# Optimization experiments

Measured on AMD Instinct MI355X. Metric: run time of the kernel, lower is better.

The kernel has to match this reference:

```python
import jax, jax.numpy as jnp
import numpy as np
from jax import lax

N, T, CH, EMB, H, C = 256, 87, 21, 50, 128, 43  # utterances, max tokens, chars, glove dim, gru hidden, classes


def setup_inputs() -> dict:
    key = jax.random.key(0)
    ks = iter(jax.random.split(key, 40))
    def rn(shape, s=0.1):
        return (jax.random.normal(next(ks), shape) * s).astype(jnp.float32)
    return {
        "token_embeddings": rn((N, T, EMB), 1.0),
        "token_char_embeddings": rn((N, T, CH, EMB), 1.0),
        "conv1_w": rn((T, T, 5, 5)), "conv1_b": rn((T,)),
        "conv2_w": rn((T, T, 5, 5)), "conv2_b": rn((T,)),
        "utt_wih_f": rn((3 * H, 58)), "utt_whh_f": rn((3 * H, H)),
        "utt_bih_f": rn((3 * H,)), "utt_bhh_f": rn((3 * H,)),
        "utt_wih_b": rn((3 * H, 58)), "utt_whh_b": rn((3 * H, H)),
        "utt_bih_b": rn((3 * H,)), "utt_bhh_b": rn((3 * H,)),
        "ctx_w1": rn((H, 2 * H)), "ctx_w2": rn((H, H)), "ctx_b2": rn((H,)), "ctx_w3": rn((H, H)),
        "proj_w": rn((1, 2 * H)), "proj_b": rn((1,)),
        "gx0": rn((2, 2, H)),
        "cg_wih_f": rn((3 * H, 1)), "cg_whh_f": rn((3 * H, H)),
        "cg_bih_f": rn((3 * H,)), "cg_bhh_f": rn((3 * H,)),
        "cg_wih_b": rn((3 * H, 1)), "cg_whh_b": rn((3 * H, H)),
        "cg_bih_b": rn((3 * H,)), "cg_bhh_b": rn((3 * H,)),
        "cls_w1": rn((2 * H, 4 * H)), "cls_b1": rn((2 * H,)),
        "cls_w2": rn((H, 2 * H)), "cls_b2": rn((H,)),
        "cls_w3": rn((C, H)), "cls_b3": rn((C,)),
    }


def gru_cell(x, h, wih, whh, bih, bhh):
    # torch nn.GRU gate order: r, z, n
    gi = x @ wih.T + bih
    gh = h @ whh.T + bhh
    ir, iz, in_ = jnp.split(gi, 3, axis=-1)
    hr, hz, hn = jnp.split(gh, 3, axis=-1)
    r = jax.nn.sigmoid(ir + hr)
    z = jax.nn.sigmoid(iz + hz)
    n = jnp.tanh(in_ + r * hn)
    return (1.0 - z) * n + z * h


def gru_last(x_tbd, h0, wih, whh, bih, bhh):
    # x_tbd: [T, B, D] time-major; returns final hidden [B, H]
    def step(h, xt):
        return gru_cell(xt, h, wih, whh, bih, bhh), None
    hT, _ = lax.scan(step, h0, x_tbd)
    return hT


def _forward(token_embeddings, token_char_embeddings, conv1_w, conv1_b, conv2_w, conv2_b,
             utt_wih_f, utt_whh_f, utt_bih_f, utt_bhh_f,
             utt_wih_b, utt_whh_b, utt_bih_b, utt_bhh_b,
             ctx_w1, ctx_w2, ctx_b2, ctx_w3, proj_w, proj_b, gx0,
             cg_wih_f, cg_whh_f, cg_bih_f, cg_bhh_f,
             cg_wih_b, cg_whh_b, cg_bih_b, cg_bhh_b,
             cls_w1, cls_b1, cls_w2, cls_b2, cls_w3, cls_b3):
    def conv(x, w, b):
        y = lax.conv_general_dilated(x, w, (1, 1), 'VALID',
                                     dimension_numbers=('NCHW', 'OIHW', 'NCHW'))
        return y + b[None, :, None, None]

    def maxpool(x):
        return lax.reduce_window(x, -jnp.inf, lax.max, (1, 1, 3, 3), (1, 1, 2, 2), 'VALID')

    # utterance CNN over char embeddings: [N,87,21,50] -> [N,87,1,8]
    x = maxpool(jax.nn.relu(conv(token_char_embeddings, conv1_w, conv1_b)))
    x = maxpool(jax.nn.relu(conv(x, conv2_w, conv2_b)))
    cnn = x.reshape(x.shape[0], x.shape[1], -1)  # [N,87,8]
    rnn_in = jnp.concatenate([token_embeddings, cnn], axis=2)  # [N,87,58]

    # bidirectional utterance GRU -> final hidden states, [N,256]
    x_tm = jnp.swapaxes(rnn_in, 0, 1)  # [87,N,58]
    h0 = jnp.zeros((rnn_in.shape[0], H), dtype=rnn_in.dtype)
    hf = gru_last(x_tm, h0, utt_wih_f, utt_whh_f, utt_bih_f, utt_bhh_f)
    hb = gru_last(x_tm[::-1], h0, utt_wih_b, utt_whh_b, utt_bih_b, utt_bhh_b)
    Hall = jnp.concatenate([hf, hb], axis=1)  # [N,256]

    def conv_gru(seq, hx):
        # seq: [2,128,1] (batch=2, seq=128, feat=1); hx: [2,2,128] (dir, batch, hid)
        stm = jnp.swapaxes(seq, 0, 1)  # [128,2,1]
        hf_ = gru_last(stm, hx[0], cg_wih_f, cg_whh_f, cg_bih_f, cg_bhh_f)
        hb_ = gru_last(stm[::-1], hx[1], cg_wih_b, cg_whh_b, cg_bih_b, cg_bhh_b)
        return jnp.stack([hf_, hb_])  # [2,2,128]

    def ctx_step(gx, hx_row):
        gx_sg = lax.stop_gradient(gx)  # matches .detach() in the original
        Hx = hx_row[None, :]                        # [1,256]
        a = Hx @ ctx_w1.T                           # [1,128]
        b = gx_sg[0][:, None, :] @ ctx_w2.T + ctx_b2  # [2,1,128]
        S = jnp.tanh(a + b) @ ctx_w3.T              # [2,1,128]
        A = jax.nn.softmax(S, axis=-1)              # [2,1,128]
        Mx = A[:, 0, :, None] * Hx[0][None, None, :]  # A^T @ Hx -> [2,128,256]
        one_d = Mx @ proj_w.T + proj_b              # [2,128,1]
        new_gx = conv_gru(one_d, gx_sg)             # [2,2,128]
        return new_gx, new_gx.reshape(-1)           # feature = gx.view(1,-1) -> 512

    _, feats = lax.scan(ctx_step, gx0, Hall)  # [N,512]

    h1 = jax.nn.leaky_relu(feats @ cls_w1.T + cls_b1)
    h2 = jax.nn.leaky_relu(h1 @ cls_w2.T + cls_b2)
    return h2 @ cls_w3.T + cls_b3  # [N,43]


def reference(token_embeddings, token_char_embeddings, conv1_w, conv1_b, conv2_w, conv2_b,
              utt_wih_f, utt_whh_f, utt_bih_f, utt_bhh_f,
              utt_wih_b, utt_whh_b, utt_bih_b, utt_bhh_b,
              ctx_w1, ctx_w2, ctx_b2, ctx_w3, proj_w, proj_b, gx0,
              cg_wih_f, cg_whh_f, cg_bih_f, cg_bhh_f,
              cg_wih_b, cg_whh_b, cg_bih_b, cg_bhh_b,
              cls_w1, cls_b1, cls_w2, cls_b2, cls_w3, cls_b3):
    return _forward(token_embeddings, token_char_embeddings, conv1_w, conv1_b, conv2_w, conv2_b,
                    utt_wih_f, utt_whh_f, utt_bih_f, utt_bhh_f,
                    utt_wih_b, utt_whh_b, utt_bih_b, utt_bhh_b,
                    ctx_w1, ctx_w2, ctx_b2, ctx_w3, proj_w, proj_b, gx0,
                    cg_wih_f, cg_whh_f, cg_bih_f, cg_bhh_f,
                    cg_wih_b, cg_whh_b, cg_bih_b, cg_bhh_b,
                    cls_w1, cls_b1, cls_w2, cls_b2, cls_w3, cls_b3)
```

## Files before the change

kernel.cpp:

```cpp
#include <hip/hip_runtime.h>
#include <math.h>

#define NB   256
#define TDIM 87
#define HD   128
#define H3   384
#define NCLS 43

typedef float f32x4 __attribute__((ext_vector_type(4)));
typedef float f32x2 __attribute__((ext_vector_type(2)));

__device__ __forceinline__ float sigmoidf_(float x){ return 1.0f/(1.0f + __expf(-x)); }
__device__ __forceinline__ float tanhf_(float x){ return 1.0f - 2.0f/(1.0f + __expf(2.0f*x)); }
__device__ __forceinline__ float lrelu_(float x){ return x > 0.f ? x : 0.01f*x; }

__device__ __forceinline__ f32x4 gload4(const float* p_){
  f32x4 r;
  asm volatile("global_load_dwordx4 %0, %1, off" : "=v"(r) : "v"(p_));
  return r;
}
__device__ __forceinline__ float dot4v(float acc, f32x4 a, f32x4 b){
  acc = fmaf(a[0], b[0], acc); acc = fmaf(a[1], b[1], acc);
  acc = fmaf(a[2], b[2], acc); acc = fmaf(a[3], b[3], acc);
  return acc;
}

__global__ __launch_bounds__(256) void k_conv1(const float* __restrict__ tce,
    const float* __restrict__ w1, const float* __restrict__ b1,
    float* __restrict__ pool1){
  const int n = blockIdx.x, oc = blockIdx.y;
  __shared__ float xs[21*52];
  __shared__ float ws[32];
  __shared__ float cv[17*48];
  const int tid = threadIdx.x;
  const int oh = tid/12, owc = (tid%12)*4;
  const bool act = tid < 204;
  const float bias = b1[oc];
  float acc[4];
  #pragma unroll
  for (int j=0;j<4;j++) acc[j] = bias;
  const float* xin  = tce + (size_t)(n*TDIM)*1050;
  const float* wrow = w1  + (size_t)oc*TDIM*25;
  for (int ic=0; ic<TDIM; ++ic){
    for (int j=tid; j<1050; j+=256){ xs[(j/50)*52 + (j%50)] = xin[(size_t)ic*1050 + j]; }
    if (tid < 25) ws[tid] = wrow[ic*25 + tid];
    __syncthreads();
    if (act){
      float wreg[25];
      #pragma unroll
      for (int u=0;u<25;u++) wreg[u] = ws[u];
      #pragma unroll
      for (int r=0;r<5;r++){
        const float4* xr = (const float4*)&xs[(oh+r)*52 + owc];
        float4 v0 = xr[0], v1 = xr[1];
        float xv[8] = {v0.x,v0.y,v0.z,v0.w,v1.x,v1.y,v1.z,v1.w};
        #pragma unroll
        for (int c=0;c<5;c++){
          float w = wreg[r*5+c];
          #pragma unroll
          for (int j=0;j<4;j++) acc[j] = fmaf(w, xv[c+j], acc[j]);
        }
      }
    }
    __syncthreads();
  }
  if (act){
    #pragma unroll
    for (int j=0;j<4;j++){
      int ow = owc + j;
      if (ow < 46) cv[oh*48 + ow] = fmaxf(acc[j], 0.0f);
    }
  }
  __syncthreads();
  if (tid < 176){
    int ph = tid/22, pw = tid%22;
    float m = -1e30f;
    #pragma unroll
    for (int r=0;r<3;r++)
      #pragma unroll
      for (int c=0;c<3;c++)
        m = fmaxf(m, cv[(2*ph+r)*48 + (2*pw+c)]);
    pool1[((size_t)(n*TDIM+oc))*176 + tid] = m;
  }
}

__global__ __launch_bounds__(128) void k_conv2(const float* __restrict__ pool1,
    const float* __restrict__ w2, const float* __restrict__ b2,
    float* __restrict__ cnn){
  const int n = blockIdx.x, oc = blockIdx.y;
  __shared__ float xs[176];
  __shared__ float ws[32];
  __shared__ float cv[72];
  const int tid = threadIdx.x;
  float a = b2[oc];
  const int oh = tid/18, ow = tid%18;
  const float* xin = pool1 + (size_t)n*TDIM*176;
  const float* wr  = w2 + (size_t)oc*TDIM*25;
  for (int ic=0; ic<TDIM; ++ic){
    for (int j=tid; j<176; j+=128) xs[j] = xin[(size_t)ic*176 + j];
    if (tid < 25) ws[tid] = wr[ic*25 + tid];
    __syncthreads();
    if (tid < 72){
      #pragma unroll
      for (int r=0;r<5;r++)
        #pragma unroll
        for (int c=0;c<5;c++)
          a = fmaf(ws[r*5+c], xs[(oh+r)*22 + (ow+c)], a);
    }
    __syncthreads();
  }
  if (tid < 72) cv[tid] = fmaxf(a, 0.0f);
  __syncthreads();
  if (tid < 8){
    float m = -1e30f;
    #pragma unroll
    for (int r=0;r<3;r++)
      #pragma unroll
      for (int c=0;c<3;c++)
        m = fmaxf(m, cv[r*18 + (2*tid+c)]);
    cnn[((size_t)(n*TDIM+oc))*8 + tid] = m;
  }
}

__global__ __launch_bounds__(768,3) void k_utt(
    const float* __restrict__ te, const float* __restrict__ cnn,
    const float* __restrict__ wih_f, const float* __restrict__ whh_f,
    const float* __restrict__ bih_f, const float* __restrict__ bhh_f,
    const float* __restrict__ wih_b, const float* __restrict__ whh_b,
    const float* __restrict__ bih_b, const float* __restrict__ bhh_b,
    float* __restrict__ Hall){
  const int bx  = blockIdx.x;
  const int dir = bx & 1;
  const int n   = bx >> 1;
  const int tid = threadIdx.x;
  const int o   = tid >> 1, kh = tid & 1;
  const float* wih = dir ? wih_b : wih_f;
  const float* whh = dir ? whh_b : whh_f;
  const float* bih = dir ? bih_b : bih_f;
  const float* bhh = dir ? bhh_b : bhh_f;
  float wh[64], wi[32];
  { const float4* wp = (const float4*)(whh + (size_t)o*128 + kh*64);
    #pragma unroll
    for (int q=0;q<16;q++){ float4 v=wp[q]; wh[4*q]=v.x; wh[4*q+1]=v.y; wh[4*q+2]=v.z; wh[4*q+3]=v.w; } }
  #pragma unroll
  for (int k=0;k<32;k++){ int c = kh*32 + k; wi[k] = (c < 58) ? wih[(size_t)o*58 + c] : 0.f; }
  const float bI = bih[o], bH = bhh[o];
  __shared__ float h[128];
  __shared__ float xb[64];
  __shared__ float s_rz[256];
  __shared__ float gin_s[128];
  __shared__ float ghn_s[128];
  if (tid < 128) h[tid] = 0.f;
  if (tid < 64)  xb[tid] = 0.f;
  __syncthreads();
  for (int t=0;t<TDIM;++t){
    const int ttt = dir ? (TDIM-1-t) : t;
    if (tid < 50)      xb[tid] = te[((size_t)n*TDIM + ttt)*50 + tid];
    else if (tid < 58) xb[tid] = cnn[((size_t)n*TDIM + ttt)*8 + (tid - 50)];
    __syncthreads();
    float a0=0,a1=0,a2=0,a3=0;
    const float4* hp = (const float4*)&h[kh*64];
    #pragma unroll
    for (int q=0;q<16;q++){ float4 hv=hp[q];
      a0=fmaf(wh[4*q],hv.x,a0); a1=fmaf(wh[4*q+1],hv.y,a1);
      a2=fmaf(wh[4*q+2],hv.z,a2); a3=fmaf(wh[4*q+3],hv.w,a3); }
    float ah = (a0+a1)+(a2+a3);
    float c0=0,c1=0,c2=0,c3=0;
    const float4* xp = (const float4*)&xb[kh*32];
    #pragma unroll
    for (int q=0;q<8;q++){ float4 xv=xp[q];
      c0=fmaf(wi[4*q],xv.x,c0); c1=fmaf(wi[4*q+1],xv.y,c1);
      c2=fmaf(wi[4*q+2],xv.z,c2); c3=fmaf(wi[4*q+3],xv.w,c3); }
    float ai = (c0+c1)+(c2+c3);
    ah += __shfl_xor(ah, 1);
    ai += __shfl_xor(ai, 1);
    if (kh == 0){
      if (o < 256) s_rz[o] = ah + ai + bI + bH;
      else { gin_s[o-256] = ai + bI; ghn_s[o-256] = ah + bH; }
    }
    __syncthreads();
    if (tid < 128){
      float r  = sigmoidf_(s_rz[tid]);
      float z  = sigmoidf_(s_rz[128+tid]);
      float nn = tanhf_(gin_s[tid] + r*ghn_s[tid]);
      h[tid] = (1.f - z)*nn + z*h[tid];
    }
    __syncthreads();
  }
  if (tid < 128) Hall[(size_t)n*256 + dir*128 + tid] = h[tid];
}

__global__ __launch_bounds__(256) void k_prep(const float* __restrict__ Hall,
    const float* __restrict__ ctx_w1, const float* __restrict__ proj_w,
    float* __restrict__ a_all, float* __restrict__ s_all){
  const int i = blockIdx.x; const int tid = threadIdx.x;
  __shared__ float hr[256];
  __shared__ float red[2];
  hr[tid] = Hall[(size_t)i*256 + tid];
  __syncthreads();
  if (tid < 128){
    const float4* w  = (const float4*)(ctx_w1 + (size_t)tid*256);
    const float4* hp = (const float4*)hr;
    float a0=0,a1=0,a2=0,a3=0;
    #pragma unroll 8
    for (int q=0;q<64;q++){ float4 wv=w[q], hv=hp[q];
      a0=fmaf(wv.x,hv.x,a0); a1=fmaf(wv.y,hv.y,a1); a2=fmaf(wv.z,hv.z,a2); a3=fmaf(wv.w,hv.w,a3); }
    a_all[(size_t)i*128 + tid] = (a0+a1)+(a2+a3);
  } else {
    const int k = tid - 128;
    float p = hr[k]*proj_w[k] + hr[k+128]*proj_w[k+128];
    #pragma unroll
    for (int off=32; off; off>>=1) p += __shfl_xor(p, off);
    if ((tid & 63) == 0) red[(tid-128)>>6] = p;
  }
  __syncthreads();
  if (tid == 0) s_all[i] = red[0] + red[1];
}

__global__ __launch_bounds__(512,2) void k_ctx(
    const float* __restrict__ cg_wih_f, const float* __restrict__ cg_whh_f,
    const float* __restrict__ cg_bih_f, const float* __restrict__ cg_bhh_f,
    const float* __restrict__ cg_wih_b, const float* __restrict__ cg_whh_b,
    const float* __restrict__ cg_bih_b, const float* __restrict__ cg_bhh_b,
    const float* __restrict__ ctx_w2, const float* __restrict__ ctx_b2,
    const float* __restrict__ ctx_w3, const float* __restrict__ proj_b,
    const float* __restrict__ gx0,
    const float* __restrict__ a_all, const float* __restrict__ s_all,
    float* __restrict__ one_d_g, int* __restrict__ flags,
    float* __restrict__ feats){
  const int blk = blockIdx.x;
  const bool isF = blk < 2;
  const int d   = blk & 1;
  const int tid = threadIdx.x;
  const int p   = tid >> 2;
  const int kq  = tid & 3;
  const float* whh = isF ? cg_whh_f : cg_whh_b;
  const float* wih = isF ? cg_wih_f : cg_wih_b;
  const float* bih = isF ? cg_bih_f : cg_bih_b;
  const float* bhh = isF ? cg_bhh_f : cg_bhh_b;

  const float* wrb = whh + (size_t)(      p)*128 + kq*32;
  const float* wzb = whh + (size_t)(128 + p)*128 + kq*32;
  const float* wnb = whh + (size_t)(256 + p)*128 + kq*32;
  f32x4 wr0=gload4(wrb),    wr1=gload4(wrb+4),  wr2=gload4(wrb+8),  wr3=gload4(wrb+12);
  f32x4 wr4=gload4(wrb+16), wr5=gload4(wrb+20), wr6=gload4(wrb+24), wr7=gload4(wrb+28);
  f32x4 wz0=gload4(wzb),    wz1=gload4(wzb+4),  wz2=gload4(wzb+8),  wz3=gload4(wzb+12);
  f32x4 wz4=gload4(wzb+16), wz5=gload4(wzb+20), wz6=gload4(wzb+24), wz7=gload4(wzb+28);
  f32x4 wn0=gload4(wnb),    wn1=gload4(wnb+4),  wn2=gload4(wnb+8),  wn3=gload4(wnb+12);
  f32x4 wn4=gload4(wnb+16), wn5=gload4(wnb+20), wn6=gload4(wnb+24), wn7=gload4(wnb+28);
  asm volatile("s_waitcnt vmcnt(0)" ::: "memory");
  __builtin_amdgcn_sched_barrier(0);

  float wir = wih[p],      wiz = wih[128+p], win = wih[256+p];
  float br_ = bih[p]      + bhh[p];
  float bz_ = bih[128+p]  + bhh[128+p];
  float bn_ = bih[256+p];
  float bhn_ = bhh[256+p];
  float pb = proj_b[0];
  asm volatile("" : "+v"(wir), "+v"(wiz), "+v"(win), "+v"(br_), "+v"(bz_),
                    "+v"(bn_), "+v"(bhn_), "+v"(pb));

  __shared__ float hl[2][160];
  __shared__ float one_d_s[128];
  __shared__ float T_s[160];
  __shared__ float S_s[128];
  __shared__ float red_s[2];

  const float* gsrc = gx0 + (size_t)((isF ? 0 : 2) + d)*128;
  float hm = gsrc[p];
  if (tid < 128) hl[0][(tid>>4)*20 + (tid&15)] = gsrc[tid];
  __syncthreads();

  const int chp = (p>>4)*20 + (p&15);
  const int kb  = kq*40;

  for (int i=0;i<NB;++i){
    if (isF){
      const float* w2r = ctx_w2 + (size_t)p*128 + kq*32;
      const float* w3r = ctx_w3 + (size_t)p*128 + kq*32;
      f32x4 u0=gload4(w2r),    u1=gload4(w2r+4),  u2=gload4(w2r+8),  u3=gload4(w2r+12);
      f32x4 u4=gload4(w2r+16), u5=gload4(w2r+20), u6=gload4(w2r+24), u7=gload4(w2r+28);
      f32x4 v0=gload4(w3r),    v1=gload4(w3r+4),  v2=gload4(w3r+8),  v3=gload4(w3r+12);
      f32x4 v4=gload4(w3r+16), v5=gload4(w3r+20), v6=gload4(w3r+24), v7=gload4(w3r+28);
      asm volatile("s_waitcnt vmcnt(0)" ::: "memory");
      __builtin_amdgcn_sched_barrier(0);
      {
        const f32x4* hA = (const f32x4*)&hl[0][kb];
        const f32x4* hB = (const f32x4*)&hl[0][kb+20];
        f32x4 q0=hA[0],q1=hA[1],q2=hA[2],q3=hA[3];
        f32x4 q4=hB[0],q5=hB[1],q6=hB[2],q7=hB[3];
        float sa=0, sb=0;
        sa=dot4v(sa,u0,q0); sa=dot4v(sa,u1,q1); sa=dot4v(sa,u2,q2); sa=dot4v(sa,u3,q3);
        sb=dot4v(sb,u4,q4); sb=dot4v(sb,u5,q5); sb=dot4v(sb,u6,q6); sb=dot4v(sb,u7,q7);
        float s = sa + sb;
        s += __shfl_xor(s,1); s += __shfl_xor(s,2);
        if (kq == 0) T_s[chp] = tanhf_(a_all[(size_t)i*128 + p] + s + ctx_b2[p]);
      }
      __syncthreads();
      {
        const f32x4* tA = (const f32x4*)&T_s[kb];
        const f32x4* tB = (const f32x4*)&T_s[kb+20];
        f32x4 t0=tA[0],t1=tA[1],t2=tA[2],t3=tA[3];
        f32x4 t4=tB[0],t5=tB[1],t6=tB[2],t7=tB[3];
        float sa=0, sb=0;
        sa=dot4v(sa,v0,t0); sa=dot4v(sa,v1,t1); sa=dot4v(sa,v2,t2); sa=dot4v(sa,v3,t3);
        sb=dot4v(sb,v4,t4); sb=dot4v(sb,v5,t5); sb=dot4v(sb,v6,t6); sb=dot4v(sb,v7,t7);
        float s = sa + sb;
        s += __shfl_xor(s,1); s += __shfl_xor(s,2);
        if (kq == 0) S_s[p] = s;
      }
      __syncthreads();
      if (tid < 64){
        float m = fmaxf(S_s[tid], S_s[tid+64]);
        #pragma unroll
        for (int off=32; off; off>>=1) m = fmaxf(m, __shfl_xor(m, off));
        if (tid == 0) red_s[0] = m;
      }
      __syncthreads();
      if (tid < 128) S_s[tid] = __expf(S_s[tid] - red_s[0]);
      __syncthreads();
      if (tid < 64){
        float s = S_s[tid] + S_s[tid+64];
        #pragma unroll
        for (int off=32; off; off>>=1) s += __shfl_xor(s, off);
        if (tid == 0) red_s[1] = s;
      }
      __syncthreads();
      if (tid < 128){
        float v = (S_s[tid] / red_s[1]) * s_all[i] + pb;
        one_d_s[tid] = v;
        __hip_atomic_store(&one_d_g[((size_t)d*NB + i)*128 + tid], v,
                           __ATOMIC_RELAXED, __HIP_MEMORY_SCOPE_AGENT);
      }
      __syncthreads();
      if (tid == 0){
        __threadfence();
        __hip_atomic_store(&flags[d], i+1, __ATOMIC_RELEASE, __HIP_MEMORY_SCOPE_AGENT);
      }
    } else {
      if (tid == 0){
        while (__hip_atomic_load(&flags[d], __ATOMIC_ACQUIRE, __HIP_MEMORY_SCOPE_AGENT) < i+1){
          __builtin_amdgcn_s_sleep(8);
        }
      }
      __syncthreads();
      if (tid < 128)
        one_d_s[tid] = __hip_atomic_load(&one_d_g[((size_t)d*NB + i)*128 + tid],
                                         __ATOMIC_RELAXED, __HIP_MEMORY_SCOPE_AGENT);
      __syncthreads();
    }
    for (int tc=0; tc<128; ++tc){
      const float* hcur = hl[tc & 1];
      float*       hnxt = hl[(tc & 1) ^ 1];
      const f32x4* hA = (const f32x4*)&hcur[kb];
      const f32x4* hB = (const f32x4*)&hcur[kb+20];
      f32x4 h0=hA[0],h1=hA[1],h2=hA[2],h3=hA[3];
      f32x4 h4=hB[0],h5=hB[1],h6=hB[2],h7=hB[3];
      f32x2 ar2 = {0.f,0.f}, az2 = {0.f,0.f}, an2 = {0.f,0.f};
      ar2 += wr0.lo*h0.lo; ar2 += wr0.hi*h0.hi; ar2 += wr1.lo*h1.lo; ar2 += wr1.hi*h1.hi;
      ar2 += wr2.lo*h2.lo; ar2 += wr2.hi*h2.hi; ar2 += wr3.lo*h3.lo; ar2 += wr3.hi*h3.hi;
      ar2 += wr4.lo*h4.lo; ar2 += wr4.hi*h4.hi; ar2 += wr5.lo*h5.lo; ar2 += wr5.hi*h5.hi;
      ar2 += wr6.lo*h6.lo; ar2 += wr6.hi*h6.hi; ar2 += wr7.lo*h7.lo; ar2 += wr7.hi*h7.hi;
      az2 += wz0.lo*h0.lo; az2 += wz0.hi*h0.hi; az2 += wz1.lo*h1.lo; az2 += wz1.hi*h1.hi;
      az2 += wz2.lo*h2.lo; az2 += wz2.hi*h2.hi; az2 += wz3.lo*h3.lo; az2 += wz3.hi*h3.hi;
      az2 += wz4.lo*h4.lo; az2 += wz4.hi*h4.hi; az2 += wz5.lo*h5.lo; az2 += wz5.hi*h5.hi;
      az2 += wz6.lo*h6.lo; az2 += wz6.hi*h6.hi; az2 += wz7.lo*h7.lo; az2 += wz7.hi*h7.hi;
      an2 += wn0.lo*h0.lo; an2 += wn0.hi*h0.hi; an2 += wn1.lo*h1.lo; an2 += wn1.hi*h1.hi;
      an2 += wn2.lo*h2.lo; an2 += wn2.hi*h2.hi; an2 += wn3.lo*h3.lo; an2 += wn3.hi*h3.hi;
      an2 += wn4.lo*h4.lo; an2 += wn4.hi*h4.hi; an2 += wn5.lo*h5.lo; an2 += wn5.hi*h5.hi;
      an2 += wn6.lo*h6.lo; an2 += wn6.hi*h6.hi; an2 += wn7.lo*h7.lo; an2 += wn7.hi*h7.hi;
      float ar = ar2.x + ar2.y;
      float az = az2.x + az2.y;
      float an = an2.x + an2.y;
      ar += __shfl_xor(ar,1); ar += __shfl_xor(ar,2);
      az += __shfl_xor(az,1); az += __shfl_xor(az,2);
      an += __shfl_xor(an,1); an += __shfl_xor(an,2);
      if (kq == 0){
        float x = one_d_s[isF ? tc : 127-tc];
        float r  = sigmoidf_(fmaf(x, wir, br_) + ar);
        float z  = sigmoidf_(fmaf(x, wiz, bz_) + az);
        float nn = tanhf_(fmaf(x, win, bn_) + r*(an + bhn_));
        hm = (1.f - z)*nn + z*hm;
        hnxt[chp] = hm;
      }
      __syncthreads();
    }
    if (kq == 0){
      const int off = isF ? d*128 : 256 + d*128;
      feats[(size_t)i*512 + off + p] = hm;
    }
    __syncthreads();
  }
}

__global__ __launch_bounds__(256) void k_cls(const float* __restrict__ feats,
    const float* __restrict__ w1, const float* __restrict__ b1,
    const float* __restrict__ w2, const float* __restrict__ b2,
    const float* __restrict__ w3, const float* __restrict__ b3,
    float* __restrict__ out){
  const int n = blockIdx.x; const int tid = threadIdx.x;
  __shared__ float fr[512];
  __shared__ float h1s[256];
  __shared__ float h2s[128];
  fr[tid]       = feats[(size_t)n*512 + tid];
  fr[tid+256]   = feats[(size_t)n*512 + 256 + tid];
  __syncthreads();
  {
    const float4* w  = (const float4*)(w1 + (size_t)tid*512);
    const float4* fp = (const float4*)fr;
    float a0=0,a1=0,a2=0,a3=0;
    #pragma unroll 8
    for (int q=0;q<128;q++){ float4 wv=w[q], fv=fp[q];
      a0=fmaf(wv.x,fv.x,a0); a1=fmaf(wv.y,fv.y,a1); a2=fmaf(wv.z,fv.z,a2); a3=fmaf(wv.w,fv.w,a3); }
    h1s[tid] = lrelu_(b1[tid] + (a0+a1)+(a2+a3));
  }
  __syncthreads();
  if (tid < 128){
    const float4* w  = (const float4*)(w2 + (size_t)tid*256);
    const float4* fp = (const float4*)h1s;
    float a0=0,a1=0,a2=0,a3=0;
    #pragma unroll 8
    for (int q=0;q<64;q++){ float4 wv=w[q], fv=fp[q];
      a0=fmaf(wv.x,fv.x,a0); a1=fmaf(wv.y,fv.y,a1); a2=fmaf(wv.z,fv.z,a2); a3=fmaf(wv.w,fv.w,a3); }
    h2s[tid] = lrelu_(b2[tid] + (a0+a1)+(a2+a3));
  }
  __syncthreads();
  if (tid < NCLS){
    const float4* w  = (const float4*)(w3 + (size_t)tid*128);
    const float4* fp = (const float4*)h2s;
    float a0=0,a1=0,a2=0,a3=0;
    #pragma unroll 8
    for (int q=0;q<32;q++){ float4 wv=w[q], fv=fp[q];
      a0=fmaf(wv.x,fv.x,a0); a1=fmaf(wv.y,fv.y,a1); a2=fmaf(wv.z,fv.z,a2); a3=fmaf(wv.w,fv.w,a3); }
    out[(size_t)n*NCLS + tid] = b3[tid] + (a0+a1)+(a2+a3);
  }
}

#define OFF_FLAGS  0u
#define OFF_SALL   512u
#define OFF_AALL   2048u
#define OFF_ONED   133632u
#define OFF_HALL   395776u
#define OFF_FEATS  657920u
#define OFF_CNN    1182208u
#define OFF_POOL1  1894912u

extern "C" void kernel_launch(void* const* d_in, const int* in_sizes, int n_in,
                              void* d_out, int out_size, void* d_ws, size_t ws_size,
                              hipStream_t stream){
  const float* te   = (const float*)d_in[0];
  const float* tce  = (const float*)d_in[1];
  const float* c1w  = (const float*)d_in[2];
  const float* c1b  = (const float*)d_in[3];
  const float* c2w  = (const float*)d_in[4];
  const float* c2b  = (const float*)d_in[5];
  const float* uwif = (const float*)d_in[6];
  const float* uwhf = (const float*)d_in[7];
  const float* ubif = (const float*)d_in[8];
  const float* ubhf = (const float*)d_in[9];
  const float* uwib = (const float*)d_in[10];
  const float* uwhb = (const float*)d_in[11];
  const float* ubib = (const float*)d_in[12];
  const float* ubhb = (const float*)d_in[13];
  const float* cw1  = (const float*)d_in[14];
  const float* cw2  = (const float*)d_in[15];
  const float* cb2  = (const float*)d_in[16];
  const float* cw3  = (const float*)d_in[17];
  const float* pw   = (const float*)d_in[18];
  const float* pbb  = (const float*)d_in[19];
  const float* gx0  = (const float*)d_in[20];
  const float* gwif = (const float*)d_in[21];
  const float* gwhf = (const float*)d_in[22];
  const float* gbif = (const float*)d_in[23];
  const float* gbhf = (const float*)d_in[24];
  const float* gwib = (const float*)d_in[25];
  const float* gwhb = (const float*)d_in[26];
  const float* gbib = (const float*)d_in[27];
  const float* gbhb = (const float*)d_in[28];
  const float* clw1 = (const float*)d_in[29];
  const float* clb1 = (const float*)d_in[30];
  const float* clw2 = (const float*)d_in[31];
  const float* clb2 = (const float*)d_in[32];
  const float* clw3 = (const float*)d_in[33];
  const float* clb3 = (const float*)d_in[34];
  float* out = (float*)d_out;
  char* ws = (char*)d_ws;
  int*   flags = (int*)  (ws + OFF_FLAGS);
  float* s_all = (float*)(ws + OFF_SALL);
  float* a_all = (float*)(ws + OFF_AALL);
  float* one_d = (float*)(ws + OFF_ONED);
  float* Hall  = (float*)(ws + OFF_HALL);
  float* feats = (float*)(ws + OFF_FEATS);
  float* cnn   = (float*)(ws + OFF_CNN);
  float* pool1 = (float*)(ws + OFF_POOL1);

  hipMemsetAsync(flags, 0, 64, stream);
  k_conv1<<<dim3(NB, TDIM), 256, 0, stream>>>(tce, c1w, c1b, pool1);
  k_conv2<<<dim3(NB, TDIM), 128, 0, stream>>>(pool1, c2w, c2b, cnn);
  k_utt<<<512, 768, 0, stream>>>(te, cnn, uwif, uwhf, ubif, ubhf,
                                 uwib, uwhb, ubib, ubhb, Hall);
  k_prep<<<NB, 256, 0, stream>>>(Hall, cw1, pw, a_all, s_all);
  k_ctx<<<4, 512, 0, stream>>>(gwif, gwhf, gbif, gbhf, gwib, gwhb, gbib, gbhb,
                               cw2, cb2, cw3, pbb, gx0, a_all, s_all,
                               one_d, flags, feats);
  k_cls<<<NB, 256, 0, stream>>>(feats, clw1, clb1, clw2, clb2, clw3, clb3, out);
}
```

Baseline: 24.21 ms.

## Merge context GRU batch rows into two blocks using fp16 dot2 recurrence

The context GRU kernel now runs two blocks instead of four. Each block handles both batch rows (dd=0,1) of its direction, processing them together in one interleaved recurrence loop. Recurrent weights and hidden state are held in fp16 and the matvecs use packed fdot2 instructions. This halves register pressure for the weights and shares barriers across both rows, with the aim of cutting per-step latency in the serial 256x128 loop. In exchange it risks fp16 precision error in the hidden state and serialises the forward block's two softmax computations.

```diff
diff --git a/kernel.cpp b/kernel.cpp
--- a/kernel.cpp
+++ b/kernel.cpp
@@ -8,7 +8,8 @@
 #define NCLS 43
 
 typedef float f32x4 __attribute__((ext_vector_type(4)));
-typedef float f32x2 __attribute__((ext_vector_type(2)));
+typedef _Float16 f16x8 __attribute__((ext_vector_type(8)));
+typedef _Float16 f16x2 __attribute__((ext_vector_type(2)));
 
 __device__ __forceinline__ float sigmoidf_(float x){ return 1.0f/(1.0f + __expf(-x)); }
 __device__ __forceinline__ float tanhf_(float x){ return 1.0f - 2.0f/(1.0f + __expf(2.0f*x)); }
@@ -23,6 +24,25 @@
   acc = fmaf(a[0], b[0], acc); acc = fmaf(a[1], b[1], acc);
   acc = fmaf(a[2], b[2], acc); acc = fmaf(a[3], b[3], acc);
   return acc;
+}
+__device__ __forceinline__ float dot8h(float acc, f16x8 a, f16x8 b){
+  f16x2 a0={a[0],a[1]}, a1={a[2],a[3]}, a2={a[4],a[5]}, a3={a[6],a[7]};
+  f16x2 b0={b[0],b[1]}, b1={b[2],b[3]}, b2={b[4],b[5]}, b3={b[6],b[7]};
+  acc = __builtin_amdgcn_fdot2(a0,b0,acc,false);
+  acc = __builtin_amdgcn_fdot2(a1,b1,acc,false);
+  acc = __builtin_amdgcn_fdot2(a2,b2,acc,false);
+  acc = __builtin_amdgcn_fdot2(a3,b3,acc,false);
+  return acc;
+}
+__device__ __forceinline__ f16x8 cvt8h(const float* p){
+  f16x8 r;
+  #pragma unroll
+  for (int j=0;j<8;j++) r[j] = (_Float16)p[j];
+  return r;
+}
+__device__ __forceinline__ void h8tof(f16x8 a, f32x4& lo, f32x4& hi){
+  lo[0]=(float)a[0]; lo[1]=(float)a[1]; lo[2]=(float)a[2]; lo[3]=(float)a[3];
+  hi[0]=(float)a[4]; hi[1]=(float)a[5]; hi[2]=(float)a[6]; hi[3]=(float)a[7];
 }
 
 __global__ __launch_bounds__(256) void k_conv1(const float* __restrict__ tce,
@@ -228,9 +248,7 @@
     const float* __restrict__ a_all, const float* __restrict__ s_all,
     float* __restrict__ one_d_g, int* __restrict__ flags,
     float* __restrict__ feats){
-  const int blk = blockIdx.x;
-  const bool isF = blk < 2;
-  const int d   = blk & 1;
+  const bool isF = (blockIdx.x == 0);
   const int tid = threadIdx.x;
   const int p   = tid >> 2;
   const int kq  = tid & 3;
@@ -242,14 +260,12 @@
   const float* wrb = whh + (size_t)(      p)*128 + kq*32;
   const float* wzb = whh + (size_t)(128 + p)*128 + kq*32;
   const float* wnb = whh + (size_t)(256 + p)*128 + kq*32;
-  f32x4 wr0=gload4(wrb),    wr1=gload4(wrb+4),  wr2=gload4(wrb+8),  wr3=gload4(wrb+12);
-  f32x4 wr4=gload4(wrb+16), wr5=gload4(wrb+20), wr6=gload4(wrb+24), wr7=gload4(wrb+28);
-  f32x4 wz0=gload4(wzb),    wz1=gload4(wzb+4),  wz2=gload4(wzb+8),  wz3=gload4(wzb+12);
-  f32x4 wz4=gload4(wzb+16), wz5=gload4(wzb+20), wz6=gload4(wzb+24), wz7=gload4(wzb+28);
-  f32x4 wn0=gload4(wnb),    wn1=gload4(wnb+4),  wn2=gload4(wnb+8),  wn3=gload4(wnb+12);
-  f32x4 wn4=gload4(wnb+16), wn5=gload4(wnb+20), wn6=gload4(wnb+24), wn7=gload4(wnb+28);
-  asm volatile("s_waitcnt vmcnt(0)" ::: "memory");
-  __builtin_amdgcn_sched_barrier(0);
+  f16x8 wr0=cvt8h(wrb), wr1=cvt8h(wrb+8), wr2=cvt8h(wrb+16), wr3=cvt8h(wrb+24);
+  f16x8 wz0=cvt8h(wzb), wz1=cvt8h(wzb+8), wz2=cvt8h(wzb+16), wz3=cvt8h(wzb+24);
+  f16x8 wn0=cvt8h(wnb), wn1=cvt8h(wnb+8), wn2=cvt8h(wnb+16), wn3=cvt8h(wnb+24);
+  asm volatile("" : "+v"(wr0), "+v"(wr1), "+v"(wr2), "+v"(wr3),
+                    "+v"(wz0), "+v"(wz1), "+v"(wz2), "+v"(wz3),
+                    "+v"(wn0), "+v"(wn1), "+v"(wn2), "+v"(wn3));
 
   float wir = wih[p],      wiz = wih[128+p], win = wih[256+p];
   float br_ = bih[p]      + bhh[p];
@@ -260,19 +276,24 @@
   asm volatile("" : "+v"(wir), "+v"(wiz), "+v"(win), "+v"(br_), "+v"(bz_),
                     "+v"(bn_), "+v"(bhn_), "+v"(pb));
 
-  __shared__ float hl[2][160];
-  __shared__ float one_d_s[128];
+  __shared__ _Float16 hl16[2][2][160];
+  __shared__ float one_d_s[2][128];
   __shared__ float T_s[160];
   __shared__ float S_s[128];
   __shared__ float red_s[2];
 
-  const float* gsrc = gx0 + (size_t)((isF ? 0 : 2) + d)*128;
-  float hm = gsrc[p];
-  if (tid < 128) hl[0][(tid>>4)*20 + (tid&15)] = gsrc[tid];
-  __syncthreads();
-
-  const int chp = (p>>4)*20 + (p&15);
-  const int kb  = kq*40;
+  const int gbase = isF ? 0 : 2;
+  float hm0 = gx0[(size_t)(gbase+0)*128 + p];
+  float hm1 = gx0[(size_t)(gbase+1)*128 + p];
+  if (tid < 128){
+    int slot = ((tid>>5)*40) + (tid&31);
+    hl16[0][0][slot] = (_Float16)gx0[(size_t)(gbase+0)*128 + tid];
+    hl16[1][0][slot] = (_Float16)gx0[(size_t)(gbase+1)*128 + tid];
+  }
+  __syncthreads();
+
+  const int chp  = ((p>>5)*40) + (p&31);
+  const int kb16 = kq*40;
 
   for (int i=0;i<NB;++i){
     if (isF){
@@ -284,110 +305,124 @@
       f32x4 v4=gload4(w3r+16), v5=gload4(w3r+20), v6=gload4(w3r+24), v7=gload4(w3r+28);
       asm volatile("s_waitcnt vmcnt(0)" ::: "memory");
       __builtin_amdgcn_sched_barrier(0);
-      {
-        const f32x4* hA = (const f32x4*)&hl[0][kb];
-        const f32x4* hB = (const f32x4*)&hl[0][kb+20];
-        f32x4 q0=hA[0],q1=hA[1],q2=hA[2],q3=hA[3];
-        f32x4 q4=hB[0],q5=hB[1],q6=hB[2],q7=hB[3];
-        float sa=0, sb=0;
-        sa=dot4v(sa,u0,q0); sa=dot4v(sa,u1,q1); sa=dot4v(sa,u2,q2); sa=dot4v(sa,u3,q3);
-        sb=dot4v(sb,u4,q4); sb=dot4v(sb,u5,q5); sb=dot4v(sb,u6,q6); sb=dot4v(sb,u7,q7);
-        float s = sa + sb;
-        s += __shfl_xor(s,1); s += __shfl_xor(s,2);
-        if (kq == 0) T_s[chp] = tanhf_(a_all[(size_t)i*128 + p] + s + ctx_b2[p]);
+      #pragma unroll
+      for (int dd=0; dd<2; ++dd){
+        {
+          const f16x8* hp0 = (const f16x8*)&hl16[dd][0][kb16];
+          f16x8 a0=hp0[0], a1=hp0[1], a2=hp0[2], a3=hp0[3];
+          f32x4 g0,g1,g2,g3,g4,g5,g6,g7;
+          h8tof(a0,g0,g1); h8tof(a1,g2,g3); h8tof(a2,g4,g5); h8tof(a3,g6,g7);
+          float s=0;
+          s=dot4v(s,u0,g0); s=dot4v(s,u1,g1); s=dot4v(s,u2,g2); s=dot4v(s,u3,g3);
+          s=dot4v(s,u4,g4); s=dot4v(s,u5,g5); s=dot4v(s,u6,g6); s=dot4v(s,u7,g7);
+          s += __shfl_xor(s,1); s += __shfl_xor(s,2);
+          if (kq == 0) T_s[((p>>4)*20)+(p&15)] = tanhf_(a_all[(size_t)i*128 + p] + s + ctx_b2[p]);
+        }
+        __syncthreads();
+        {
+          const f32x4* tA = (const f32x4*)&T_s[kq*40];
+          const f32x4* tB = (const f32x4*)&T_s[kq*40+20];
+          f32x4 t0=tA[0],t1=tA[1],t2=tA[2],t3=tA[3];
+          f32x4 t4=tB[0],t5=tB[1],t6=tB[2],t7=tB[3];
+          float s=0;
+          s=dot4v(s,v0,t0); s=dot4v(s,v1,t1); s=dot4v(s,v2,t2); s=dot4v(s,v3,t3);
+          s=dot4v(s,v4,t4); s=dot4v(s,v5,t5); s=dot4v(s,v6,t6); s=dot4v(s,v7,t7);
+          s += __shfl_xor(s,1); s += __shfl_xor(s,2);
+          if (kq == 0) S_s[p] = s;
+        }
+        __syncthreads();
+        if (tid < 64){
+          float m = fmaxf(S_s[tid], S_s[tid+64]);
+          #pragma unroll
+          for (int off=32; off; off>>=1) m = fmaxf(m, __shfl_xor(m, off));
+          if (tid == 0) red_s[0] = m;
+        }
+        __syncthreads();
+        if (tid < 128) S_s[tid] = __expf(S_s[tid] - red_s[0]);
+        __syncthreads();
+        if (tid < 64){
+          float s = S_s[tid] + S_s[tid+64];
+          #pragma unroll
+          for (int off=32; off; off>>=1) s += __shfl_xor(s, off);
+          if (tid == 0) red_s[1] = s;
+        }
+        __syncthreads();
+        if (tid < 128){
+          float v = (S_s[tid] / red_s[1]) * s_all[i] + pb;
+          one_d_s[dd][tid] = v;
+          __hip_atomic_store(&one_d_g[((size_t)dd*NB + i)*128 + tid], v,
+                             __ATOMIC_RELAXED, __HIP_MEMORY_SCOPE_AGENT);
+        }
+        __syncthreads();
       }
-      __syncthreads();
-      {
-        const f32x4* tA = (const f32x4*)&T_s[kb];
-        const f32x4* tB = (const f32x4*)&T_s[kb+20];
-        f32x4 t0=tA[0],t1=tA[1],t2=tA[2],t3=tA[3];
-        f32x4 t4=tB[0],t5=tB[1],t6=tB[2],t7=tB[3];
-        float sa=0, sb=0;
-        sa=dot4v(sa,v0,t0); sa=dot4v(sa,v1,t1); sa=dot4v(sa,v2,t2); sa=dot4v(sa,v3,t3);
-        sb=dot4v(sb,v4,t4); sb=dot4v(sb,v5,t5); sb=dot4v(sb,v6,t6); sb=dot4v(sb,v7,t7);
-        float s = sa + sb;
-        s += __shfl_xor(s,1); s += __shfl_xor(s,2);
-        if (kq == 0) S_s[p] = s;
+      if (tid == 0){
+        __threadfence();
+        __hip_atomic_store(&flags[0], i+1, __ATOMIC_RELEASE, __HIP_MEMORY_SCOPE_AGENT);
       }
-      __syncthreads();
-      if (tid < 64){
-        float m = fmaxf(S_s[tid], S_s[tid+64]);
-        #pragma unroll
-        for (int off=32; off; off>>=1) m = fmaxf(m, __shfl_xor(m, off));
-        if (tid == 0) red_s[0] = m;
-      }
-      __syncthreads();
-      if (tid < 128) S_s[tid] = __expf(S_s[tid] - red_s[0]);
-      __syncthreads();
-      if (tid < 64){
-        float s = S_s[tid] + S_s[tid+64];
-        #pragma unroll
-        for (int off=32; off; off>>=1) s += __shfl_xor(s, off);
-        if (tid == 0) red_s[1] = s;
+    } else {
+      if (tid == 0){
+        while (__hip_atomic_load(&flags[0], __ATOMIC_ACQUIRE, __HIP_MEMORY_SCOPE_AGENT) < i+1){
+          __builtin_amdgcn_s_sleep(8);
+        }
       }
       __syncthreads();
       if (tid < 128){
-        float v = (S_s[tid] / red_s[1]) * s_all[i] + pb;
-        one_d_s[tid] = v;
-        __hip_atomic_store(&one_d_g[((size_t)d*NB + i)*128 + tid], v,
-                           __ATOMIC_RELAXED, __HIP_MEMORY_SCOPE_AGENT);
+        one_d_s[0][tid] = __hip_atomic_load(&one_d_g[((size_t)0*NB + i)*128 + tid],
+                                            __ATOMIC_RELAXED, __HIP_MEMORY_SCOPE_AGENT);
+        one_d_s[1][tid] = __hip_atomic_load(&one_d_g[((size_t)1*NB + i)*128 + tid],
+                                            __ATOMIC_RELAXED, __HIP_MEMORY_SCOPE_AGENT);
       }
       __syncthreads();
-      if (tid == 0){
-        __threadfence();
-        __hip_atomic_store(&flags[d], i+1, __ATOMIC_RELEASE, __HIP_MEMORY_SCOPE_AGENT);
-      }
-    } else {
-      if (tid == 0){
-        while (__hip_atomic_load(&flags[d], __ATOMIC_ACQUIRE, __HIP_MEMORY_SCOPE_AGENT) < i+1){
-          __builtin_amdgcn_s_sleep(8);
-        }
+    }
+    for (int tc=0; tc<128; ++tc){
+      const _Float16* hc0 = hl16[0][tc & 1];
+      const _Float16* hc1 = hl16[1][tc & 1];
+      _Float16* hn0 = hl16[0][(tc & 1) ^ 1];
+      _Float16* hn1 = hl16[1][(tc & 1) ^ 1];
+      const f16x8* hp0 = (const f16x8*)&hc0[kb16];
+      const f16x8* hp1 = (const f16x8*)&hc1[kb16];
+      f16x8 a0=hp0[0], a1=hp0[1], a2=hp0[2], a3=hp0[3];
+      f16x8 b0=hp1[0], b1=hp1[1], b2=hp1[2], b3=hp1[3];
+      float ar0=0, az0=0, an0=0, ar1=0, az1=0, an1=0;
+      ar0=dot8h(ar0,wr0,a0); ar1=dot8h(ar1,wr0,b0);
+      ar0=dot8h(ar0,wr1,a1); ar1=dot8h(ar1,wr1,b1);
+      ar0=dot8h(ar0,wr2,a2); ar1=dot8h(ar1,wr2,b2);
+      ar0=dot8h(ar0,wr3,a3); ar1=dot8h(ar1,wr3,b3);
+      az0=dot8h(az0,wz0,a0); az1=dot8h(az1,wz0,b0);
+      az0=dot8h(az0,wz1,a1); az1=dot8h(az1,wz1,b1);
+      az0=dot8h(az0,wz2,a2); az1=dot8h(az1,wz2,b2);
+      az0=dot8h(az0,wz3,a3); az1=dot8h(az1,wz3,b3);
+      an0=dot8h(an0,wn0,a0); an1=dot8h(an1,wn0,b0);
+      an0=dot8h(an0,wn1,a1); an1=dot8h(an1,wn1,b1);
+      an0=dot8h(an0,wn2,a2); an1=dot8h(an1,wn2,b2);
+      an0=dot8h(an0,wn3,a3); an1=dot8h(an1,wn3,b3);
+      ar0 += __shfl_xor(ar0,1); ar1 += __shfl_xor(ar1,1);
+      az0 += __shfl_xor(az0,1); az1 += __shfl_xor(az1,1);
+      an0 += __shfl_xor(an0,1); an1 += __shfl_xor(an1,1);
+      ar0 += __shfl_xor(ar0,2); ar1 += __shfl_xor(ar1,2);
+      az0 += __shfl_xor(az0,2); az1 += __shfl_xor(az1,2);
+      an0 += __shfl_xor(an0,2); an1 += __shfl_xor(an1,2);
+      if (kq == 0){
+        const int xi = isF ? tc : 127-tc;
+        float x0 = one_d_s[0][xi];
+        float x1 = one_d_s[1][xi];
+        float r  = sigmoidf_(fmaf(x0, wir, br_) + ar0);
+        float z  = sigmoidf_(fmaf(x0, wiz, bz_) + az0);
+        float nn = tanhf_(fmaf(x0, win, bn_) + r*(an0 + bhn_));
+        hm0 = (1.f - z)*nn + z*hm0;
+        hn0[chp] = (_Float16)hm0;
+        r  = sigmoidf_(fmaf(x1, wir, br_) + ar1);
+        z  = sigmoidf_(fmaf(x1, wiz, bz_) + az1);
+        nn = tanhf_(fmaf(x1, win, bn_) + r*(an1 + bhn_));
+        hm1 = (1.f - z)*nn + z*hm1;
+        hn1[chp] = (_Float16)hm1;
       }
       __syncthreads();
-      if (tid < 128)
-        one_d_s[tid] = __hip_atomic_load(&one_d_g[((size_t)d*NB + i)*128 + tid],
-                                         __ATOMIC_RELAXED, __HIP_MEMORY_SCOPE_AGENT);
-      __syncthreads();
-    }
-    for (int tc=0; tc<128; ++tc){
-      const float* hcur = hl[tc & 1];
-      float*       hnxt = hl[(tc & 1) ^ 1];
-      const f32x4* hA = (const f32x4*)&hcur[kb];
-      const f32x4* hB = (const f32x4*)&hcur[kb+20];
-      f32x4 h0=hA[0],h1=hA[1],h2=hA[2],h3=hA[3];
-      f32x4 h4=hB[0],h5=hB[1],h6=hB[2],h7=hB[3];
-      f32x2 ar2 = {0.f,0.f}, az2 = {0.f,0.f}, an2 = {0.f,0.f};
-      ar2 += wr0.lo*h0.lo; ar2 += wr0.hi*h0.hi; ar2 += wr1.lo*h1.lo; ar2 += wr1.hi*h1.hi;
-      ar2 += wr2.lo*h2.lo; ar2 += wr2.hi*h2.hi; ar2 += wr3.lo*h3.lo; ar2 += wr3.hi*h3.hi;
-      ar2 += wr4.lo*h4.lo; ar2 += wr4.hi*h4.hi; ar2 += wr5.lo*h5.lo; ar2 += wr5.hi*h5.hi;
-      ar2 += wr6.lo*h6.lo; ar2 += wr6.hi*h6.hi; ar2 += wr7.lo*h7.lo; ar2 += wr7.hi*h7.hi;
-      az2 += wz0.lo*h0.lo; az2 += wz0.hi*h0.hi; az2 += wz1.lo*h1.lo; az2 += wz1.hi*h1.hi;
-      az2 += wz2.lo*h2.lo; az2 += wz2.hi*h2.hi; az2 += wz3.lo*h3.lo; az2 += wz3.hi*h3.hi;
-      az2 += wz4.lo*h4.lo; az2 += wz4.hi*h4.hi; az2 += wz5.lo*h5.lo; az2 += wz5.hi*h5.hi;
-      az2 += wz6.lo*h6.lo; az2 += wz6.hi*h6.hi; az2 += wz7.lo*h7.lo; az2 += wz7.hi*h7.hi;
-      an2 += wn0.lo*h0.lo; an2 += wn0.hi*h0.hi; an2 += wn1.lo*h1.lo; an2 += wn1.hi*h1.hi;
-      an2 += wn2.lo*h2.lo; an2 += wn2.hi*h2.hi; an2 += wn3.lo*h3.lo; an2 += wn3.hi*h3.hi;
-      an2 += wn4.lo*h4.lo; an2 += wn4.hi*h4.hi; an2 += wn5.lo*h5.lo; an2 += wn5.hi*h5.hi;
-      an2 += wn6.lo*h6.lo; an2 += wn6.hi*h6.hi; an2 += wn7.lo*h7.lo; an2 += wn7.hi*h7.hi;
-      float ar = ar2.x + ar2.y;
-      float az = az2.x + az2.y;
-      float an = an2.x + an2.y;
-      ar += __shfl_xor(ar,1); ar += __shfl_xor(ar,2);
-      az += __shfl_xor(az,1); az += __shfl_xor(az,2);
-      an += __shfl_xor(an,1); an += __shfl_xor(an,2);
-      if (kq == 0){
-        float x = one_d_s[isF ? tc : 127-tc];
-        float r  = sigmoidf_(fmaf(x, wir, br_) + ar);
-        float z  = sigmoidf_(fmaf(x, wiz, bz_) + az);
-        float nn = tanhf_(fmaf(x, win, bn_) + r*(an + bhn_));
-        hm = (1.f - z)*nn + z*hm;
-        hnxt[chp] = hm;
-      }
-      __syncthreads();
     }
     if (kq == 0){
-      const int off = isF ? d*128 : 256 + d*128;
-      feats[(size_t)i*512 + off + p] = hm;
+      const int base = isF ? 0 : 256;
+      feats[(size_t)i*512 + base + 0*128 + p] = hm0;
+      feats[(size_t)i*512 + base + 1*128 + p] = hm1;
     }
     __syncthreads();
   }
@@ -500,7 +535,7 @@
   k_utt<<<512, 768, 0, stream>>>(te, cnn, uwif, uwhf, ubif, ubhf,
                                  uwib, uwhb, ubib, ubhb, Hall);
   k_prep<<<NB, 256, 0, stream>>>(Hall, cw1, pw, a_all, s_all);
-  k_ctx<<<4, 512, 0, stream>>>(gwif, gwhf, gbif, gbhf, gwib, gwhb, gbib, gbhb,
+  k_ctx<<<2, 512, 0, stream>>>(gwif, gwhf, gbif, gbhf, gwib, gwhb, gbib, gbhb,
                                cw2, cb2, cw3, pbb, gx0, a_all, s_all,
                                one_d, flags, feats);
   k_cls<<<NB, 256, 0, stream>>>(feats, clw1, clb1, clw2, clb2, clw3, clb3, out);
```

New measurement: 41.82 ms. 1.73x slower.
